# Optimization experiments

Hardware: AMD Instinct MI355X
Metric: run time of the kernel (lower is better)

## Reference

```python
import jax, jax.numpy as jnp
import numpy as np

N_HEADS = 16
HIDDEN = 1024
HEAD_SIZE = HIDDEN // N_HEADS  # 64
BATCH = 2
SEQ_LEN = 2048


def setup_inputs() -> dict:
    key = jax.random.key(0)
    k1, k2, k3 = jax.random.split(key, 3)
    x = jax.random.normal(k1, (BATCH, SEQ_LEN, HIDDEN), dtype=jnp.float32)
    # nn.Linear(hidden, 3*hidden): store weight as [in, out] for x @ W
    W_qkv = jax.random.normal(k2, (HIDDEN, 3 * HIDDEN), dtype=jnp.float32) * (HIDDEN ** -0.5)
    b_qkv = jax.random.normal(k3, (3 * HIDDEN,), dtype=jnp.float32) * 0.02
    return {"x": x, "W_qkv": W_qkv, "b_qkv": b_qkv}


def reference(x, W_qkv, b_qkv):
    B, T, D = x.shape
    nh, hs = N_HEADS, HEAD_SIZE
    scale = hs ** -0.5

    # qkv projection, then the module's exact (unusual) reshape:
    # [B,T,3D] viewed as [3,B,T,hs,nh], permuted to [3,B,nh,T,hs]
    y = x @ W_qkv + b_qkv                      # [B, T, 3D]
    qkv = y.reshape(3, B, T, hs, nh).transpose(0, 1, 4, 2, 3)  # [3,B,nh,T,hs]
    q, k, v = qkv[0], qkv[1], qkv[2]

    # KV-cache scatter with arange index over the full seq is an identity write;
    # cache.transpose(1,2) returns k, v unchanged.

    scores = jnp.einsum('bhtd,bhsd->bhts', q, k) * scale       # [B,nh,T,T]
    causal = jnp.tril(jnp.ones((T, T), dtype=bool))
    scores = jnp.where(causal[None, None], scores, -jnp.inf)
    attn = jax.nn.softmax(scores, axis=-1)
    ctx = jnp.einsum('bhts,bhsd->bhtd', attn, v)               # [B,nh,T,hs]
    # rearrange 'b h t d -> b t (h d)'; note self.o is NOT applied in forward
    return ctx.transpose(0, 2, 1, 3).reshape(B, T, nh * hs)
```

## Files before the change

### kernel.cpp

```cpp
#include <hip/hip_runtime.h>
#include <hip/hip_bf16.h>

typedef __attribute__((ext_vector_type(8))) short s8v;
typedef __attribute__((ext_vector_type(4))) short s4v;
typedef __attribute__((ext_vector_type(4))) float f4v;

__device__ __forceinline__ void g2lds16(const void* g, void* l) {
  __builtin_amdgcn_global_load_lds(
      (__attribute__((address_space(1))) void*)(g),
      (__attribute__((address_space(3))) void*)(l), 16, 0, 0);
}

__device__ __forceinline__ short f2bf(float f) {
  __hip_bfloat16 h = __float2bfloat16(f);
  return *reinterpret_cast<short*>(&h);
}

__global__ void k_prep(const float* __restrict__ x, const float* __restrict__ W,
                       __hip_bfloat16* __restrict__ xb, __hip_bfloat16* __restrict__ Wt) {
  int bx = blockIdx.x;
  if (bx < 4096) {
    int i = (bx * 256 + threadIdx.x) * 4;
    float4 v = *(const float4*)(x + i);
    __hip_bfloat16 o[4] = {__float2bfloat16(v.x), __float2bfloat16(v.y),
                           __float2bfloat16(v.z), __float2bfloat16(v.w)};
    *(uint2*)(xb + i) = *(const uint2*)(o);
  } else {
    __shared__ float tile[32][33];
    int r = bx - 4096;
    int rt = r / 96;
    int ct = r - rt * 96;
    int c0 = ct * 32, r0 = rt * 32;
    int tr = threadIdx.x >> 5, tc = threadIdx.x & 31;
#pragma unroll
    for (int i = 0; i < 32; i += 8)
      tile[tr + i][tc] = W[(size_t)(r0 + tr + i) * 3072 + c0 + tc];
    __syncthreads();
#pragma unroll
    for (int i = 0; i < 32; i += 8)
      Wt[(size_t)(c0 + tr + i) * 1024 + r0 + tc] = __float2bfloat16(tile[tc][tr + i]);
  }
}

__global__ __launch_bounds__(256) void k_gemm(const __hip_bfloat16* __restrict__ A,
                                              const __hip_bfloat16* __restrict__ Bt,
                                              const float* __restrict__ bias,
                                              __hip_bfloat16* __restrict__ Q,
                                              __hip_bfloat16* __restrict__ K,
                                              __hip_bfloat16* __restrict__ Vt) {
  __shared__ __align__(16) __hip_bfloat16 As[2][128 * 32];
  __shared__ __align__(16) __hip_bfloat16 Bs[2][128 * 32];
  const int tid = threadIdx.x;
  const int lane = tid & 63, wave = tid >> 6;
  const int m0 = blockIdx.y * 128, n0 = blockIdx.x * 128;
  const int wm = (wave & 1) * 64, wn = (wave >> 1) * 64;
  const int lrow = lane & 15;
  const int quad = lane >> 4;

  f4v acc[4][4] = {};

  auto stage = [&](int k0, int kb) {
#pragma unroll
    for (int c = 0; c < 2; ++c) {
      int e = c * 2048 + tid * 8;
      int row = e >> 5;
      int slot = (e & 31) >> 3;
      int src = k0 + ((slot ^ ((row >> 1) & 3)) << 3);
      g2lds16(A + (size_t)(m0 + row) * 1024 + src, &As[kb][e]);
      g2lds16(Bt + (size_t)(n0 + row) * 1024 + src, &Bs[kb][e]);
    }
  };

  const int swz = (quad ^ ((lrow >> 1) & 3)) * 8;

  stage(0, 0);
  for (int it = 0; it < 32; ++it) {
    __syncthreads();
    if (it < 31) stage((it + 1) * 32, (it + 1) & 1);
    const __hip_bfloat16* Ab = As[it & 1];
    const __hip_bfloat16* Bb = Bs[it & 1];
    s8v af[4], bfr[4];
#pragma unroll
    for (int mi = 0; mi < 4; ++mi) af[mi] = *(const s8v*)(Ab + (wm + mi * 16 + lrow) * 32 + swz);
#pragma unroll
    for (int ni = 0; ni < 4; ++ni) bfr[ni] = *(const s8v*)(Bb + (wn + ni * 16 + lrow) * 32 + swz);
#pragma unroll
    for (int mi = 0; mi < 4; ++mi)
#pragma unroll
      for (int ni = 0; ni < 4; ++ni)
        acc[mi][ni] = __builtin_amdgcn_mfma_f32_16x16x32_bf16(af[mi], bfr[ni], acc[mi][ni], 0, 0, 0);
  }

  const int cw = n0 + wn;
  const int c10 = cw >> 10;
  const int d0 = (cw & 1023) >> 4;
  const int h = lrow;
  float bv[4];
#pragma unroll
  for (int ni = 0; ni < 4; ++ni) bv[ni] = bias[cw + ni * 16 + lrow];

#pragma unroll
  for (int mi = 0; mi < 4; ++mi) {
    int rbase = m0 + wm + mi * 16 + quad * 4;
#pragma unroll
    for (int reg = 0; reg < 4; ++reg) {
      int rr = rbase + reg;
      int u = 3 * rr + c10;
      int s = u >> 12;
      int b = (u >> 11) & 1;
      int t = u & 2047;
      if (s < 2) {
        __hip_bfloat16* dst = (s == 0) ? Q : K;
        const float qs = (s == 0) ? 0.18033688011112042f : 1.0f;
        s4v pk;
#pragma unroll
        for (int ni = 0; ni < 4; ++ni) pk[ni] = f2bf((acc[mi][ni][reg] + bv[ni]) * qs);
        *(s4v*)(dst + ((size_t)(b * 16 + h) * 2048 + t) * 64 + d0) = pk;
      } else {
#pragma unroll
        for (int ni = 0; ni < 4; ++ni)
          Vt[((size_t)(b * 16 + h) * 64 + d0 + ni) * 2048 + t] =
              __float2bfloat16(acc[mi][ni][reg] + bv[ni]);
      }
    }
  }
}

__global__ __launch_bounds__(256, 2) void k_attn(const __hip_bfloat16* __restrict__ Q,
                                                 const __hip_bfloat16* __restrict__ K,
                                                 const __hip_bfloat16* __restrict__ Vt,
                                                 float* __restrict__ out) {
  __shared__ __align__(16) char lds[2][16384];

  const int tid = threadIdx.x;
  const int lane = tid & 63, w = tid >> 6;
  const int l = lane & 15, q = lane >> 4, lx = l & 7;

  const int bid = blockIdx.x;
  const int xcd = bid & 7;
  const int idx = bid >> 3;
  const int bh = xcd + 8 * (idx & 3);
  const int kk = 15 - (idx >> 2);
  const int qA = 2 * kk, qB = 2 * kk + 1;

  const char* Kb = (const char*)(K + (size_t)bh * 131072);
  const char* Vb = (const char*)(Vt + (size_t)bh * 131072);
  const __hip_bfloat16* QpA = Q + (size_t)bh * 131072 + (size_t)qA * 4096;
  const __hip_bfloat16* QpB = Q + (size_t)bh * 131072 + (size_t)qB * 4096;

  s8v QfA[2], QfB[2];
#pragma unroll
  for (int kh = 0; kh < 2; ++kh) {
    QfA[kh] = *(const s8v*)(QpA + (size_t)(w * 16 + l) * 64 + kh * 32 + q * 8);
    QfB[kh] = *(const s8v*)(QpB + (size_t)(w * 16 + l) * 64 + kh * 32 + q * 8);
  }

  f4v OA[4] = {}, OB[4] = {};
  float mA = -INFINITY, lsA = 0.f;
  float mB = -INFINITY, lsB = 0.f;
  const int tgA = qA * 64 + w * 16 + l;
  const int tgB = qB * 64 + w * 16 + l;

  auto stage = [&](int j, char* buf) {
#pragma unroll
    for (int c = 0; c < 4; ++c) {
      int chunk = w * 4 + c;
      int ls = chunk * 64 + lane;
      if (chunk < 8) {
        int row = ls >> 3, kb = ls & 7;
        g2lds16(Kb + (size_t)j * 8192 + row * 128 + ((kb ^ (row & 7)) << 4),
                buf + ls * 16);
      } else {
        int ls2 = ls - 512;
        int d = ls2 >> 3, kb = ls2 & 7;
        g2lds16(Vb + (size_t)d * 4096 + (size_t)j * 128 + ((kb ^ (d & 7)) << 4),
                buf + 8192 + ls2 * 16);
      }
    }
  };

  stage(0, lds[0]);
  __syncthreads();

  for (int j = 0; j <= qB; ++j) {
    const char* Kl = lds[j & 1];
    const char* Vl = Kl + 8192;
    if (j < qB) stage(j + 1, lds[(j + 1) & 1]);

    f4v SA[4], SB[4];
#pragma unroll
    for (int nt = 0; nt < 4; ++nt) {
      const char* rowp = Kl + (nt * 16 + l) * 128;
      s8v k0 = *(const s8v*)(rowp + ((q ^ lx) << 4));
      s8v k1 = *(const s8v*)(rowp + (((4 + q) ^ lx) << 4));
      f4v zA = {0.f, 0.f, 0.f, 0.f};
      zA = __builtin_amdgcn_mfma_f32_16x16x32_bf16(k0, QfA[0], zA, 0, 0, 0);
      zA = __builtin_amdgcn_mfma_f32_16x16x32_bf16(k1, QfA[1], zA, 0, 0, 0);
      f4v zB = {0.f, 0.f, 0.f, 0.f};
      zB = __builtin_amdgcn_mfma_f32_16x16x32_bf16(k0, QfB[0], zB, 0, 0, 0);
      zB = __builtin_amdgcn_mfma_f32_16x16x32_bf16(k1, QfB[1], zB, 0, 0, 0);
      SA[nt] = zA;
      SB[nt] = zB;
    }

    if (j >= qA) {
#pragma unroll
      for (int nt = 0; nt < 4; ++nt)
#pragma unroll
        for (int r = 0; r < 4; ++r)
          if (j * 64 + nt * 16 + q * 4 + r > tgA) SA[nt][r] = -1e30f;
    }
    if (j == qB) {
#pragma unroll
      for (int nt = 0; nt < 4; ++nt)
#pragma unroll
        for (int r = 0; r < 4; ++r)
          if (j * 64 + nt * 16 + q * 4 + r > tgB) SB[nt][r] = -1e30f;
    }

    float mxA = SA[0][0], mxB = SB[0][0];
#pragma unroll
    for (int nt = 0; nt < 4; ++nt)
#pragma unroll
      for (int r = 0; r < 4; ++r) {
        mxA = fmaxf(mxA, SA[nt][r]);
        mxB = fmaxf(mxB, SB[nt][r]);
      }
    mxA = fmaxf(mxA, __shfl_xor(mxA, 16));
    mxB = fmaxf(mxB, __shfl_xor(mxB, 16));
    mxA = fmaxf(mxA, __shfl_xor(mxA, 32));
    mxB = fmaxf(mxB, __shfl_xor(mxB, 32));

    if (!__all(mxA - mA <= 8.f)) {
      float mn = fmaxf(mA, mxA);
      float alpha = exp2f(mA - mn);
      mA = mn;
      lsA *= alpha;
#pragma unroll
      for (int dt = 0; dt < 4; ++dt) OA[dt] *= alpha;
    }
    if (!__all(mxB - mB <= 8.f)) {
      float mn = fmaxf(mB, mxB);
      float alpha = exp2f(mB - mn);
      mB = mn;
      lsB *= alpha;
#pragma unroll
      for (int dt = 0; dt < 4; ++dt) OB[dt] *= alpha;
    }

    float rsA = 0.f, rsB = 0.f;
    s4v PfA[4], PfB[4];
#pragma unroll
    for (int nt = 0; nt < 4; ++nt)
#pragma unroll
      for (int r = 0; r < 4; ++r) {
        float eA = exp2f(SA[nt][r] - mA);
        float eB = exp2f(SB[nt][r] - mB);
        rsA += eA;
        rsB += eB;
        PfA[nt][r] = f2bf(eA);
        PfB[nt][r] = f2bf(eB);
      }
    rsA += __shfl_xor(rsA, 16);
    rsB += __shfl_xor(rsB, 16);
    rsA += __shfl_xor(rsA, 32);
    rsB += __shfl_xor(rsB, 32);
    lsA += rsA;
    lsB += rsB;

#pragma unroll
    for (int sc = 0; sc < 4; ++sc) {
      int so = ((sc * 2 + (q >> 1)) ^ lx) * 16 + (q & 1) * 8;
#pragma unroll
      for (int dt = 0; dt < 4; ++dt) {
        s4v vv = *(const s4v*)(Vl + (dt * 16 + l) * 128 + so);
        OA[dt] = __builtin_amdgcn_mfma_f32_16x16x16bf16_1k(vv, PfA[sc], OA[dt], 0, 0, 0);
        OB[dt] = __builtin_amdgcn_mfma_f32_16x16x16bf16_1k(vv, PfB[sc], OB[dt], 0, 0, 0);
      }
    }
    __syncthreads();
  }

  float invA = 1.f / lsA, invB = 1.f / lsB;
  int b = bh >> 4, h = bh & 15;
  float* obA = out + ((size_t)b * 2048 + tgA) * 1024 + h * 64;
  float* obB = out + ((size_t)b * 2048 + tgB) * 1024 + h * 64;
#pragma unroll
  for (int dt = 0; dt < 4; ++dt) {
    f4v vA = OA[dt] * invA;
    f4v vB = OB[dt] * invB;
    *(f4v*)(obA + dt * 16 + q * 4) = vA;
    *(f4v*)(obB + dt * 16 + q * 4) = vB;
  }
}

extern "C" void kernel_launch(void* const* d_in, const int* in_sizes, int n_in,
                              void* d_out, int out_size, void* d_ws, size_t ws_size,
                              hipStream_t stream) {
  const float* x = (const float*)d_in[0];
  const float* W = (const float*)d_in[1];
  const float* bias = (const float*)d_in[2];
  float* out = (float*)d_out;

  char* ws = (char*)d_ws;
  __hip_bfloat16* xb = (__hip_bfloat16*)ws;
  __hip_bfloat16* Wt = (__hip_bfloat16*)(ws + 8388608);
  __hip_bfloat16* Qg = (__hip_bfloat16*)(ws + 14680064);
  __hip_bfloat16* Kg = (__hip_bfloat16*)(ws + 23068672);
  __hip_bfloat16* Vt = (__hip_bfloat16*)(ws + 31457280);

  k_prep<<<7168, 256, 0, stream>>>(x, W, xb, Wt);
  k_gemm<<<dim3(24, 32), 256, 0, stream>>>(xb, Wt, bias, Qg, Kg, Vt);
  k_attn<<<512, 256, 0, stream>>>(Qg, Kg, Vt, out);
}
```

Baseline: 185.7 us.

## Pair short and long causal query tiles per block to balance work

Each block now processes query tile kk together with tile 31-kk instead of two adjacent tiles, so every block covers the same number of causal key tiles. Work for tile A is skipped once the key index passes its diagonal, using wave-uniform branches. Before, blocks with late tile pairs ran far longer than blocks with early ones. The per-iteration branches add some control overhead and could weaken instruction scheduling.

```diff
diff --git a/kernel.cpp b/kernel.cpp
--- a/kernel.cpp
+++ b/kernel.cpp
@@ -140,8 +140,8 @@
   const int xcd = bid & 7;
   const int idx = bid >> 3;
   const int bh = xcd + 8 * (idx & 3);
-  const int kk = 15 - (idx >> 2);
-  const int qA = 2 * kk, qB = 2 * kk + 1;
+  const int kk = idx >> 2;
+  const int qA = kk, qB = 31 - kk;
 
   const char* Kb = (const char*)(K + (size_t)bh * 131072);
   const char* Vb = (const char*)(Vt + (size_t)bh * 131072);
@@ -186,6 +186,7 @@
     const char* Kl = lds[j & 1];
     const char* Vl = Kl + 8192;
     if (j < qB) stage(j + 1, lds[(j + 1) & 1]);
+    const bool actA = (j <= qA);
 
     f4v SA[4], SB[4];
 #pragma unroll
@@ -193,23 +194,18 @@
       const char* rowp = Kl + (nt * 16 + l) * 128;
       s8v k0 = *(const s8v*)(rowp + ((q ^ lx) << 4));
       s8v k1 = *(const s8v*)(rowp + (((4 + q) ^ lx) << 4));
-      f4v zA = {0.f, 0.f, 0.f, 0.f};
-      zA = __builtin_amdgcn_mfma_f32_16x16x32_bf16(k0, QfA[0], zA, 0, 0, 0);
-      zA = __builtin_amdgcn_mfma_f32_16x16x32_bf16(k1, QfA[1], zA, 0, 0, 0);
       f4v zB = {0.f, 0.f, 0.f, 0.f};
       zB = __builtin_amdgcn_mfma_f32_16x16x32_bf16(k0, QfB[0], zB, 0, 0, 0);
       zB = __builtin_amdgcn_mfma_f32_16x16x32_bf16(k1, QfB[1], zB, 0, 0, 0);
-      SA[nt] = zA;
       SB[nt] = zB;
-    }
-
-    if (j >= qA) {
-#pragma unroll
-      for (int nt = 0; nt < 4; ++nt)
-#pragma unroll
-        for (int r = 0; r < 4; ++r)
-          if (j * 64 + nt * 16 + q * 4 + r > tgA) SA[nt][r] = -1e30f;
-    }
+      if (actA) {
+        f4v zA = {0.f, 0.f, 0.f, 0.f};
+        zA = __builtin_amdgcn_mfma_f32_16x16x32_bf16(k0, QfA[0], zA, 0, 0, 0);
+        zA = __builtin_amdgcn_mfma_f32_16x16x32_bf16(k1, QfA[1], zA, 0, 0, 0);
+        SA[nt] = zA;
+      }
+    }
+
     if (j == qB) {
 #pragma unroll
       for (int nt = 0; nt < 4; ++nt)
@@ -218,27 +214,13 @@
           if (j * 64 + nt * 16 + q * 4 + r > tgB) SB[nt][r] = -1e30f;
     }
 
-    float mxA = SA[0][0], mxB = SB[0][0];
+    float mxB = SB[0][0];
 #pragma unroll
     for (int nt = 0; nt < 4; ++nt)
 #pragma unroll
-      for (int r = 0; r < 4; ++r) {
-        mxA = fmaxf(mxA, SA[nt][r]);
-        mxB = fmaxf(mxB, SB[nt][r]);
-      }
-    mxA = fmaxf(mxA, __shfl_xor(mxA, 16));
+      for (int r = 0; r < 4; ++r) mxB = fmaxf(mxB, SB[nt][r]);
     mxB = fmaxf(mxB, __shfl_xor(mxB, 16));
-    mxA = fmaxf(mxA, __shfl_xor(mxA, 32));
     mxB = fmaxf(mxB, __shfl_xor(mxB, 32));
-
-    if (!__all(mxA - mA <= 8.f)) {
-      float mn = fmaxf(mA, mxA);
-      float alpha = exp2f(mA - mn);
-      mA = mn;
-      lsA *= alpha;
-#pragma unroll
-      for (int dt = 0; dt < 4; ++dt) OA[dt] *= alpha;
-    }
     if (!__all(mxB - mB <= 8.f)) {
       float mn = fmaxf(mB, mxB);
       float alpha = exp2f(mB - mn);
@@ -247,26 +229,64 @@
 #pragma unroll
       for (int dt = 0; dt < 4; ++dt) OB[dt] *= alpha;
     }
-
-    float rsA = 0.f, rsB = 0.f;
-    s4v PfA[4], PfB[4];
-#pragma unroll
-    for (int nt = 0; nt < 4; ++nt)
-#pragma unroll
-      for (int r = 0; r < 4; ++r) {
-        float eA = exp2f(SA[nt][r] - mA);
-        float eB = exp2f(SB[nt][r] - mB);
-        rsA += eA;
-        rsB += eB;
-        PfA[nt][r] = f2bf(eA);
-        PfB[nt][r] = f2bf(eB);
-      }
-    rsA += __shfl_xor(rsA, 16);
-    rsB += __shfl_xor(rsB, 16);
-    rsA += __shfl_xor(rsA, 32);
-    rsB += __shfl_xor(rsB, 32);
-    lsA += rsA;
-    lsB += rsB;
+    float rsB = 0.f;
+    s4v PfB[4];
+    s4v PfA[4];
+    float rsA = 0.f;
+
+    if (actA) {
+      if (j == qA) {
+#pragma unroll
+        for (int nt = 0; nt < 4; ++nt)
+#pragma unroll
+          for (int r = 0; r < 4; ++r)
+            if (j * 64 + nt * 16 + q * 4 + r > tgA) SA[nt][r] = -1e30f;
+      }
+      float mxA = SA[0][0];
+#pragma unroll
+      for (int nt = 0; nt < 4; ++nt)
+#pragma unroll
+        for (int r = 0; r < 4; ++r) mxA = fmaxf(mxA, SA[nt][r]);
+      mxA = fmaxf(mxA, __shfl_xor(mxA, 16));
+      mxA = fmaxf(mxA, __shfl_xor(mxA, 32));
+      if (!__all(mxA - mA <= 8.f)) {
+        float mn = fmaxf(mA, mxA);
+        float alpha = exp2f(mA - mn);
+        mA = mn;
+        lsA *= alpha;
+#pragma unroll
+        for (int dt = 0; dt < 4; ++dt) OA[dt] *= alpha;
+      }
+#pragma unroll
+      for (int nt = 0; nt < 4; ++nt)
+#pragma unroll
+        for (int r = 0; r < 4; ++r) {
+          float eA = exp2f(SA[nt][r] - mA);
+          float eB = exp2f(SB[nt][r] - mB);
+          rsA += eA;
+          rsB += eB;
+          PfA[nt][r] = f2bf(eA);
+          PfB[nt][r] = f2bf(eB);
+        }
+      rsA += __shfl_xor(rsA, 16);
+      rsB += __shfl_xor(rsB, 16);
+      rsA += __shfl_xor(rsA, 32);
+      rsB += __shfl_xor(rsB, 32);
+      lsA += rsA;
+      lsB += rsB;
+    } else {
+#pragma unroll
+      for (int nt = 0; nt < 4; ++nt)
+#pragma unroll
+        for (int r = 0; r < 4; ++r) {
+          float eB = exp2f(SB[nt][r] - mB);
+          rsB += eB;
+          PfB[nt][r] = f2bf(eB);
+        }
+      rsB += __shfl_xor(rsB, 16);
+      rsB += __shfl_xor(rsB, 32);
+      lsB += rsB;
+    }
 
 #pragma unroll
     for (int sc = 0; sc < 4; ++sc) {
@@ -274,8 +294,9 @@
 #pragma unroll
       for (int dt = 0; dt < 4; ++dt) {
         s4v vv = *(const s4v*)(Vl + (dt * 16 + l) * 128 + so);
-        OA[dt] = __builtin_amdgcn_mfma_f32_16x16x16bf16_1k(vv, PfA[sc], OA[dt], 0, 0, 0);
         OB[dt] = __builtin_amdgcn_mfma_f32_16x16x16bf16_1k(vv, PfB[sc], OB[dt], 0, 0, 0);
+        if (actA)
+          OA[dt] = __builtin_amdgcn_mfma_f32_16x16x16bf16_1k(vv, PfA[sc], OA[dt], 0, 0, 0);
       }
     }
     __syncthreads();
```

Result: slower. 219.2 us (+18.0%).
